# Performance work log

Hardware: AMD Instinct MI355X
Metric: run time of the kernel (lower is better)

The kernel has to match this reference:

```python
import jax, jax.numpy as jnp
import numpy as np
from jax.scipy.linalg import expm

D = 512      # d_model
S = 3        # num_scales
BATCH = 256
H = 8        # attention heads
HD = D // H  # head dim


def layernorm(x, g, b, eps=1e-5):
    m = jnp.mean(x, axis=-1, keepdims=True)
    v = jnp.var(x, axis=-1, keepdims=True)
    return (x - m) / jnp.sqrt(v + eps) * g + b


def setup_inputs() -> dict:
    key = jax.random.key(0)
    ks = jax.random.split(key, 16)
    sd = 1.0 / np.sqrt(D)
    inp = {
        'x': jax.random.normal(ks[0], (BATCH, D), jnp.float32),
        'h_prev': jax.random.normal(ks[1], (BATCH, D), jnp.float32),
        'lstm_h': jax.random.normal(ks[2], (S, BATCH, D), jnp.float32) * 0.1,
        'lstm_c': jax.random.normal(ks[3], (S, BATCH, D), jnp.float32) * 0.1,
        'A': jax.random.normal(ks[4], (D, D), jnp.float32) * sd,
        'Bm': jax.random.normal(ks[5], (D, D), jnp.float32) * sd,
        'dn_w1': jax.random.normal(ks[6], (D, D), jnp.float32) * sd,
        'dn_b1': jnp.zeros((D,), jnp.float32),
        'dn_g': jnp.ones((D,), jnp.float32),
        'dn_beta': jnp.zeros((D,), jnp.float32),
        'dn_w2': jax.random.normal(ks[7], (1, D), jnp.float32) * sd,
        'dn_b2': jnp.zeros((1,), jnp.float32),
        'lstm_wih': jax.random.normal(ks[8], (S, 4 * D, D), jnp.float32) * sd,
        'lstm_whh': jax.random.normal(ks[9], (S, 4 * D, D), jnp.float32) * sd,
        'lstm_bih': jnp.zeros((S, 4 * D), jnp.float32),
        'lstm_bhh': jnp.zeros((S, 4 * D), jnp.float32),
        'decays': jnp.linspace(0.5, 0.95, S, dtype=jnp.float32),
        'attn_in_w': jax.random.normal(ks[10], (3 * D, D), jnp.float32) * sd,
        'attn_in_b': jnp.zeros((3 * D,), jnp.float32),
        'attn_out_w': jax.random.normal(ks[11], (D, D), jnp.float32) * sd,
        'attn_out_b': jnp.zeros((D,), jnp.float32),
        'proj_w': jax.random.normal(ks[12], (D, (S + 2) * D), jnp.float32) * (1.0 / np.sqrt((S + 2) * D)),
        'proj_b': jnp.zeros((D,), jnp.float32),
        'proj_g': jnp.ones((D,), jnp.float32),
        'proj_beta': jnp.zeros((D,), jnp.float32),
    }
    return inp


def reference(x, h_prev, lstm_h, lstm_c, A, Bm, dn_w1, dn_b1, dn_g, dn_beta,
              dn_w2, dn_b2, lstm_wih, lstm_whh, lstm_bih, lstm_bhh, decays,
              attn_in_w, attn_in_b, attn_out_w, attn_out_b,
              proj_w, proj_b, proj_g, proj_beta):
    # ---- delta_net: Linear -> LayerNorm -> GELU(exact) -> Linear -> Softplus ----
    h1 = layernorm(x @ dn_w1.T + dn_b1, dn_g, dn_beta)
    h1 = jax.nn.gelu(h1, approximate=False)
    delta = jax.nn.softplus(h1 @ dn_w2.T + dn_b2)           # (B, 1)

    # ---- SSM update: h_t = expm(delta*A) h_prev + delta*B x ----
    A_disc = jax.vmap(expm)(delta[:, :, None] * A)          # (B, D, D)
    h_ssm = jnp.einsum('bij,bj->bi', A_disc, h_prev) + delta * jnp.einsum('ij,bj->bi', Bm, x)

    # ---- multi-scale LSTM cells (vectorized over scales) ----
    gates = (jnp.einsum('bd,skd->sbk', x, lstm_wih)
             + jnp.einsum('sbd,skd->sbk', lstm_h, lstm_whh)
             + (lstm_bih + lstm_bhh)[:, None, :])           # (S, B, 4D)
    gi, gf, gg, go = jnp.split(gates, 4, axis=-1)
    i_g = jax.nn.sigmoid(gi)
    f_g = jax.nn.sigmoid(gf)
    g_g = jnp.tanh(gg)
    o_g = jax.nn.sigmoid(go)
    c_raw = f_g * lstm_c + i_g * g_g                        # (S, B, D)
    h_new = o_g * jnp.tanh(c_raw)                           # (S, B, D)
    dec = decays[:, None, None]
    c_new = dec * lstm_c + (1.0 - dec) * c_raw              # (S, B, D)

    # ---- fusion attention: 1 query (h_ssm), S keys/values (h_new) ----
    Wq, Wk, Wv = jnp.split(attn_in_w, 3, axis=0)
    bq, bk, bv = jnp.split(attn_in_b, 3, axis=0)
    kv = jnp.transpose(h_new, (1, 0, 2))                    # (B, S, D)
    q = (h_ssm @ Wq.T + bq).reshape(-1, 1, H, HD).transpose(0, 2, 1, 3)   # (B,H,1,HD)
    k = (kv @ Wk.T + bk).reshape(-1, S, H, HD).transpose(0, 2, 1, 3)      # (B,H,S,HD)
    v = (kv @ Wv.T + bv).reshape(-1, S, H, HD).transpose(0, 2, 1, 3)
    scores = jnp.einsum('bhqe,bhke->bhqk', q, k) / np.sqrt(HD)
    attn = jax.nn.softmax(scores, axis=-1)
    ctx = jnp.einsum('bhqk,bhke->bhqe', attn, v)            # (B,H,1,HD)
    ctx = ctx.transpose(0, 2, 1, 3).reshape(-1, D)          # (B, D)
    fused = ctx @ attn_out_w.T + attn_out_b                 # (B, D)

    # ---- output projection over concat [h_ssm, fused, h_1..h_S] ----
    combined = jnp.concatenate([h_ssm, fused] + [h_new[i] for i in range(S)], axis=-1)
    output = layernorm(combined @ proj_w.T + proj_b, proj_g, proj_beta)
    return (output, h_ssm, h_new, c_new)
```

## Files before the change

kernel.cpp:

```cpp
#include <hip/hip_runtime.h>
#include <math.h>

#define DIM 512
#define NB 256
#define KMAX 16

using bf16x8 = __attribute__((ext_vector_type(8))) short;
using f32x4  = __attribute__((ext_vector_type(4))) float;
using float4v = __attribute__((ext_vector_type(4))) float;
using ushort4v = __attribute__((ext_vector_type(4))) unsigned short;

__device__ __forceinline__ unsigned short f2b(float f) {
    union { float f; unsigned int u; } v; v.f = f;
    unsigned int r = v.u + 0x7fffu + ((v.u >> 16) & 1u);
    return (unsigned short)(r >> 16);
}
__device__ __forceinline__ float b2f(unsigned short u) {
    union { unsigned int u; float f; } v; v.u = ((unsigned int)u) << 16;
    return v.f;
}
__device__ __forceinline__ ushort4v f2b4(float4v v) {
    ushort4v o;
    o.x = f2b(v.x); o.y = f2b(v.y); o.z = f2b(v.z); o.w = f2b(v.w);
    return o;
}

__device__ __forceinline__ void block_reduce2(float& s, float& q, float* sb1, float* sb2)
{
    int tid = threadIdx.x;
    #pragma unroll
    for (int off = 32; off > 0; off >>= 1) {
        s += __shfl_down(s, off);
        q += __shfl_down(q, off);
    }
    if ((tid & 63) == 0) { sb1[tid >> 6] = s; sb2[tid >> 6] = q; }
    __syncthreads();
    s = sb1[0] + sb1[1] + sb1[2] + sb1[3];
    q = sb2[0] + sb2[1] + sb2[2] + sb2[3];
    __syncthreads();
}

struct GemmDesc {
    const unsigned short* X;
    const unsigned short* W;
    const float* bias;
    float* Cf;
    unsigned short* Cb;
    unsigned short* Ct;
    int M, N, K, ldX, ldW, ldC, tr_row0, acc;
};
struct GemmArgs { GemmDesc d[5]; };
struct LnParams {
    const float* pre; const float* g; const float* beta;
    const float* w2; const float* b2; float* delta; float* coeff;
    int lnd_y;
};

__global__ __launch_bounds__(256) void gemm_mfma(GemmArgs args, LnParams lp)
{
    __shared__ unsigned short lsA[2][4096];
    __shared__ unsigned short lsB[2][4096];
    __shared__ float sb1[4], sb2[4];

    if ((int)blockIdx.y == lp.lnd_y) {
        int b = blockIdx.x, tid = threadIdx.x;
        int i0 = tid, i1 = tid + 256;
        float x0 = lp.pre[(size_t)b * DIM + i0];
        float x1 = lp.pre[(size_t)b * DIM + i1];
        float s = x0 + x1, q = x0 * x0 + x1 * x1;
        block_reduce2(s, q, sb1, sb2);
        float mean = s * (1.f / DIM);
        float var  = q * (1.f / DIM) - mean * mean;
        float inv  = rsqrtf(var + 1e-5f);
        float y0 = (x0 - mean) * inv * lp.g[i0] + lp.beta[i0];
        float y1 = (x1 - mean) * inv * lp.g[i1] + lp.beta[i1];
        float h0 = 0.5f * y0 * (1.f + erff(y0 * 0.70710678118654752f));
        float h1 = 0.5f * y1 * (1.f + erff(y1 * 0.70710678118654752f));
        float p = h0 * lp.w2[i0] + h1 * lp.w2[i1];
        float dummy = 0.f;
        block_reduce2(p, dummy, sb1, sb2);
        if (tid == 0) {
            float z = p + lp.b2[0];
            float d = (z > 20.f) ? z : log1pf(expf(z));
            lp.delta[b] = d;
            float c = 1.f;
            lp.coeff[b] = 1.f;
            for (int k = 1; k <= KMAX; ++k) { c *= d / (float)k; lp.coeff[k * 256 + b] = c; }
        }
        return;
    }

    GemmDesc de = args.d[blockIdx.y];
    int tn = de.N >> 6;
    int tiles = (de.M >> 6) * tn;
    int t = blockIdx.x;
    if (t >= tiles) return;
    int m0 = (t / tn) << 6;
    int n0 = (t % tn) << 6;

    int tid = threadIdx.x;
    int w = tid >> 6;
    int l = tid & 63;
    int nkt = de.K >> 6;

    int srow = w * 16 + (l >> 2);
    int schk = l & 3;
    const unsigned short* gA = de.X + (size_t)(m0 + srow) * de.ldX + schk * 8;
    const unsigned short* gB = de.W + (size_t)(n0 + srow) * de.ldW + schk * 8;
    unsigned short* lA = &lsA[0][(w * 64 + l) * 8];
    unsigned short* lB = &lsB[0][(w * 64 + l) * 8];

#define STAGE(bufi, kt)                                                          \
    do {                                                                         \
        __builtin_amdgcn_global_load_lds(                                        \
            (const __attribute__((address_space(1))) unsigned int*)(gA + (size_t)(kt) * 64), \
            (__attribute__((address_space(3))) unsigned int*)(lA + (bufi) * 4096), 16, 0, 0); \
        __builtin_amdgcn_global_load_lds(                                        \
            (const __attribute__((address_space(1))) unsigned int*)(gA + (size_t)(kt) * 64 + 32), \
            (__attribute__((address_space(3))) unsigned int*)(lA + (bufi) * 4096 + 2048), 16, 0, 0); \
        __builtin_amdgcn_global_load_lds(                                        \
            (const __attribute__((address_space(1))) unsigned int*)(gB + (size_t)(kt) * 64), \
            (__attribute__((address_space(3))) unsigned int*)(lB + (bufi) * 4096), 16, 0, 0); \
        __builtin_amdgcn_global_load_lds(                                        \
            (const __attribute__((address_space(1))) unsigned int*)(gB + (size_t)(kt) * 64 + 32), \
            (__attribute__((address_space(3))) unsigned int*)(lB + (bufi) * 4096 + 2048), 16, 0, 0); \
    } while (0)

    int mbase = (w >> 1) * 32;
    int nbase = (w & 1) * 32;

    f32x4 acc[2][2];
    #pragma unroll
    for (int i = 0; i < 2; ++i)
        #pragma unroll
        for (int j = 0; j < 2; ++j)
            acc[i][j] = (f32x4){0.f, 0.f, 0.f, 0.f};

    int kg = l >> 4;
    int fr = l & 15;
    int aslot = (mbase * 4 + fr * 4 + kg) * 8;
    int bslot = (nbase * 4 + fr * 4 + kg) * 8;

    STAGE(0, 0);

    for (int kt = 0; kt < nkt; ++kt) {
        __syncthreads();
        if (kt + 1 < nkt) STAGE((kt + 1) & 1, kt + 1);

        const unsigned short* bufA = &lsA[kt & 1][0];
        const unsigned short* bufB = &lsB[kt & 1][0];
        #pragma unroll
        for (int h = 0; h < 2; ++h) {
            bf16x8 a0 = *(const bf16x8*)(bufA + h * 2048 + aslot);
            bf16x8 a1 = *(const bf16x8*)(bufA + h * 2048 + aslot + 512);
            bf16x8 b0 = *(const bf16x8*)(bufB + h * 2048 + bslot);
            bf16x8 b1 = *(const bf16x8*)(bufB + h * 2048 + bslot + 512);
            acc[0][0] = __builtin_amdgcn_mfma_f32_16x16x32_bf16(a0, b0, acc[0][0], 0, 0, 0);
            acc[0][1] = __builtin_amdgcn_mfma_f32_16x16x32_bf16(a0, b1, acc[0][1], 0, 0, 0);
            acc[1][0] = __builtin_amdgcn_mfma_f32_16x16x32_bf16(a1, b0, acc[1][0], 0, 0, 0);
            acc[1][1] = __builtin_amdgcn_mfma_f32_16x16x32_bf16(a1, b1, acc[1][1], 0, 0, 0);
        }
    }

    #pragma unroll
    for (int mi = 0; mi < 2; ++mi) {
        #pragma unroll
        for (int ni = 0; ni < 2; ++ni) {
            int col = n0 + nbase + ni * 16 + fr;
            float bv = de.bias ? de.bias[col] : 0.f;
            #pragma unroll
            for (int r = 0; r < 4; ++r) {
                int row = m0 + mbase + mi * 16 + (l >> 4) * 4 + r;
                float v = acc[mi][ni][r] + bv;
                if (de.Cf) {
                    if (de.acc) de.Cf[(size_t)row * de.ldC + col] += v;
                    else        de.Cf[(size_t)row * de.ldC + col] = v;
                } else {
                    de.Cb[(size_t)row * de.ldC + col] = f2b(v);
                }
                if (de.Ct && row >= de.tr_row0)
                    de.Ct[(size_t)col * 512 + (row - de.tr_row0)] = f2b(v);
            }
        }
    }
#undef STAGE
}

#define NSEG 13
struct PrepArgs {
    const float* sA[NSEG]; const float* sB[NSEG]; unsigned short* dst[NSEG];
    int n4[NSEG], dRL4[NSEG], sRLA4[NSEG], sRLB4[NSEG], half4[NSEG], offA[NSEG];
    const float* A; unsigned short* ATb;
    const float* aout_w; unsigned short* aout_wT;
    const float* proj_w; const float* proj_b; const float* aout_b; float* bprime;
};
__global__ __launch_bounds__(256) void prep_kernel(PrepArgs a)
{
    __shared__ float tile[32][33];
    int bid = blockIdx.x, tid = threadIdx.x;
    if (bid < 2048) {
        const int gstride = 2048 * 256;
        int g0 = bid * 256 + tid;
        for (int seg = 0; seg < NSEG; ++seg) {
            int n4 = a.n4[seg];
            const float* sA = a.sA[seg];
            const float* sB = a.sB[seg];
            unsigned short* d = a.dst[seg];
            int dRL4 = a.dRL4[seg], sRLA4 = a.sRLA4[seg], sRLB4 = a.sRLB4[seg];
            int half4 = a.half4[seg], offA = a.offA[seg];
            for (int i = g0; i < n4; i += gstride) {
                int r = i / dRL4, c = i - r * dRL4;
                const float* src = (c < half4)
                    ? sA + ((size_t)r * sRLA4 + offA + c) * 4
                    : sB + ((size_t)r * sRLB4 + (c - half4)) * 4;
                float4v v = *(const float4v*)src;
                *(ushort4v*)(d + (size_t)i * 4) = f2b4(v);
            }
        }
    } else if (bid < 2560) {
        int t = bid - 2048;
        const float* src = (t < 256) ? a.A : a.aout_w;
        unsigned short* dst = (t < 256) ? a.ATb : a.aout_wT;
        int tt = t & 255;
        int bx = tt & 15, by = tt >> 4;
        int tx = tid & 31, ty = tid >> 5;
        #pragma unroll
        for (int i = 0; i < 32; i += 8)
            tile[ty + i][tx] = src[(size_t)(by * 32 + ty + i) * 512 + bx * 32 + tx];
        __syncthreads();
        #pragma unroll
        for (int i = 0; i < 32; i += 8)
            dst[(size_t)(bx * 32 + ty + i) * 512 + by * 32 + tx] = f2b(tile[tx][ty + i]);
    } else {
        int i = (bid - 2560) * 4 + (tid >> 6);
        int lane = tid & 63;
        float acc = 0.f;
        #pragma unroll
        for (int n = 0; n < 512; n += 64)
            acc += a.proj_w[(size_t)i * 2560 + 512 + n + lane] * a.aout_b[n + lane];
        #pragma unroll
        for (int off = 32; off > 0; off >>= 1) acc += __shfl_down(acc, off);
        if (lane == 0) a.bprime[i] = a.proj_b[i] + acc;
    }
}

__global__ void pointwise_fused(
    const float* __restrict__ Tm, const float* __restrict__ coeff,
    const float* __restrict__ h_prev, const float* __restrict__ delta,
    const float* __restrict__ Bx, float* __restrict__ hssm,
    unsigned short* __restrict__ combb,
    const float* __restrict__ gates, const float* __restrict__ bih,
    const float* __restrict__ bhh, const float* __restrict__ cin,
    const float* __restrict__ decays,
    float* __restrict__ hout, float* __restrict__ cout)
{
    int idx4 = blockIdx.x * 256 + threadIdx.x;
    int base = idx4 * 4;
    if (base < 131072) {
        int b = base >> 9, i = base & 511;
        const float* Tr = Tm + (size_t)b * (KMAX * DIM) + i;
        float4v a = *(const float4v*)(h_prev + base);
        #pragma unroll
        for (int k = 1; k <= KMAX; ++k) {
            float c = coeff[k * 256 + b];
            float4v t = *(const float4v*)(Tr + (size_t)(k - 1) * DIM);
            a.x += c * t.x; a.y += c * t.y; a.z += c * t.z; a.w += c * t.w;
        }
        float dl = delta[b];
        float4v bx = *(const float4v*)(Bx + base);
        a.x += dl * bx.x; a.y += dl * bx.y; a.z += dl * bx.z; a.w += dl * bx.w;
        *(float4v*)(hssm + base) = a;
        *(ushort4v*)(combb + (size_t)b * 2560 + i) = f2b4(a);
    } else {
        int i2 = base - 131072;
        int s = i2 / (NB * DIM);
        int r = i2 - s * (NB * DIM);
        int b = r >> 9, d = r & 511;
        const float* gr = gates + (size_t)s * 524288 + (size_t)b * 2048 + d;
        const float* bi = bih + s * 2048 + d;
        const float* bh = bhh + s * 2048 + d;
        float4v gi = *(const float4v*)(gr);
        float4v gf = *(const float4v*)(gr + 512);
        float4v gg = *(const float4v*)(gr + 1024);
        float4v go = *(const float4v*)(gr + 1536);
        float4v bi0 = *(const float4v*)(bi),       bh0 = *(const float4v*)(bh);
        float4v bi1 = *(const float4v*)(bi + 512), bh1 = *(const float4v*)(bh + 512);
        float4v bi2 = *(const float4v*)(bi + 1024),bh2 = *(const float4v*)(bh + 1024);
        float4v bi3 = *(const float4v*)(bi + 1536),bh3 = *(const float4v*)(bh + 1536);
        float4v c = *(const float4v*)(cin + i2);
        float dec = decays[s];
        float4v hn, cn;
        #pragma unroll
        for (int j = 0; j < 4; ++j) {
            float vgi = ((const float*)&gi)[j] + ((const float*)&bi0)[j] + ((const float*)&bh0)[j];
            float vgf = ((const float*)&gf)[j] + ((const float*)&bi1)[j] + ((const float*)&bh1)[j];
            float vgg = ((const float*)&gg)[j] + ((const float*)&bi2)[j] + ((const float*)&bh2)[j];
            float vgo = ((const float*)&go)[j] + ((const float*)&bi3)[j] + ((const float*)&bh3)[j];
            float ig = 1.f / (1.f + expf(-vgi));
            float fg = 1.f / (1.f + expf(-vgf));
            float g_ = tanhf(vgg);
            float og = 1.f / (1.f + expf(-vgo));
            float cc = ((const float*)&c)[j];
            float craw = fg * cc + ig * g_;
            ((float*)&hn)[j] = og * tanhf(craw);
            ((float*)&cn)[j] = dec * cc + (1.f - dec) * craw;
        }
        *(float4v*)(hout + i2) = hn;
        *(float4v*)(cout + i2) = cn;
        *(ushort4v*)(combb + (size_t)b * 2560 + 512 + s * 512 + d) = f2b4(hn);
    }
}

__global__ __launch_bounds__(128) void attn_kernel(
    const unsigned short* __restrict__ qb, const unsigned short* __restrict__ kvb,
    unsigned short* __restrict__ combb)
{
    int b = blockIdx.x, t = threadIdx.x;
    int h = t >> 4, sub = (t & 15) * 4;
    int col = h * 64 + sub;
    ushort4v q4 = *(const ushort4v*)(qb + (size_t)b * 512 + col);
    float qf[4] = { b2f(q4.x), b2f(q4.y), b2f(q4.z), b2f(q4.w) };
    float p[3];
    ushort4v k4[3], v4[3];
    #pragma unroll
    for (int s = 0; s < 3; ++s) {
        k4[s] = *(const ushort4v*)(kvb + (size_t)s * 262144 + (size_t)b * 1024 + col);
        v4[s] = *(const ushort4v*)(kvb + (size_t)s * 262144 + (size_t)b * 1024 + 512 + col);
        p[s] = qf[0] * b2f(k4[s].x) + qf[1] * b2f(k4[s].y)
             + qf[2] * b2f(k4[s].z) + qf[3] * b2f(k4[s].w);
    }
    #pragma unroll
    for (int off = 1; off < 16; off <<= 1) {
        p[0] += __shfl_xor(p[0], off);
        p[1] += __shfl_xor(p[1], off);
        p[2] += __shfl_xor(p[2], off);
    }
    const float scale = 0.125f;
    float p0 = p[0] * scale, p1 = p[1] * scale, p2 = p[2] * scale;
    float m = fmaxf(p0, fmaxf(p1, p2));
    float w0 = expf(p0 - m), w1 = expf(p1 - m), w2 = expf(p2 - m);
    float invs = 1.f / (w0 + w1 + w2);
    float4v ctx;
    ((float*)&ctx)[0] = (w0 * b2f(v4[0].x) + w1 * b2f(v4[1].x) + w2 * b2f(v4[2].x)) * invs;
    ((float*)&ctx)[1] = (w0 * b2f(v4[0].y) + w1 * b2f(v4[1].y) + w2 * b2f(v4[2].y)) * invs;
    ((float*)&ctx)[2] = (w0 * b2f(v4[0].z) + w1 * b2f(v4[1].z) + w2 * b2f(v4[2].z)) * invs;
    ((float*)&ctx)[3] = (w0 * b2f(v4[0].w) + w1 * b2f(v4[1].w) + w2 * b2f(v4[2].w)) * invs;
    *(ushort4v*)(combb + (size_t)b * 2560 + 2048 + col) = f2b4(ctx);
}

__global__ __launch_bounds__(256) void layernorm_k(
    const float* __restrict__ in, const float* __restrict__ g,
    const float* __restrict__ beta, float* __restrict__ outp)
{
    __shared__ float sb1[4], sb2[4];
    int b = blockIdx.x, tid = threadIdx.x;
    int i0 = tid, i1 = tid + 256;
    float x0 = in[(size_t)b * DIM + i0];
    float x1 = in[(size_t)b * DIM + i1];
    float s = x0 + x1, q = x0 * x0 + x1 * x1;
    block_reduce2(s, q, sb1, sb2);
    float mean = s * (1.f / DIM);
    float var  = q * (1.f / DIM) - mean * mean;
    float inv  = rsqrtf(var + 1e-5f);
    outp[(size_t)b * DIM + i0] = (x0 - mean) * inv * g[i0] + beta[i0];
    outp[(size_t)b * DIM + i1] = (x1 - mean) * inv * g[i1] + beta[i1];
}

extern "C" void kernel_launch(void* const* d_in, const int* in_sizes, int n_in,
                              void* d_out, int out_size, void* d_ws, size_t ws_size,
                              hipStream_t stream)
{
    const float* x        = (const float*)d_in[0];
    const float* h_prev   = (const float*)d_in[1];
    const float* lstm_h   = (const float*)d_in[2];
    const float* lstm_c   = (const float*)d_in[3];
    const float* A        = (const float*)d_in[4];
    const float* Bm       = (const float*)d_in[5];
    const float* dn_w1    = (const float*)d_in[6];
    const float* dn_b1    = (const float*)d_in[7];
    const float* dn_g     = (const float*)d_in[8];
    const float* dn_beta  = (const float*)d_in[9];
    const float* dn_w2    = (const float*)d_in[10];
    const float* dn_b2    = (const float*)d_in[11];
    const float* wih      = (const float*)d_in[12];
    const float* whh      = (const float*)d_in[13];
    const float* bih      = (const float*)d_in[14];
    const float* bhh      = (const float*)d_in[15];
    const float* decays   = (const float*)d_in[16];
    const float* ain_w    = (const float*)d_in[17];
    const float* ain_b    = (const float*)d_in[18];
    const float* aout_w   = (const float*)d_in[19];
    const float* aout_b   = (const float*)d_in[20];
    const float* proj_w   = (const float*)d_in[21];
    const float* proj_b   = (const float*)d_in[22];
    const float* proj_g   = (const float*)d_in[23];
    const float* proj_bt  = (const float*)d_in[24];

    float* out  = (float*)d_out;
    float* hssm = out + 131072;
    float* hnew = out + 262144;
    float* cnew = out + 655360;

    unsigned short* us = (unsigned short*)d_ws;
    unsigned short* hpb     = us;
    unsigned short* ATb     = us + 131072;
    unsigned short* dn_w1b  = us + 393216;
    unsigned short* Bmb     = us + 655360;
    unsigned short* ain_wb  = us + 917504;
    unsigned short* proj_wb = us + 1703936;
    unsigned short* P2b     = us + 3014656;
    unsigned short* aout_wT = us + 3276800;
    unsigned short* Pw      = us + 3538944;
    unsigned short* Qa      = us + 7733248;
    unsigned short* Qb      = us + 7995392;
    unsigned short* Wcat    = us + 8257536;
    unsigned short* Xcat    = us + 14548992;
    unsigned short* combb   = us + 15335424;
    unsigned short* qb      = us + 15990784;
    unsigned short* kvb     = us + 16121856;
    unsigned short* M2b     = us + 16908288;
    float* fbase  = (float*)(us + 17170432);
    float* pre1   = fbase;
    float* delta  = fbase + 131072;
    float* coeff  = fbase + 131328;
    float* Bx     = fbase + 135680;
    float* bprime = fbase + 266752;
    float* Tm     = fbase + 267264;
    float* gates  = fbase + 2364416;
    float* projout = pre1;

    LnParams lpOff; lpOff.pre = nullptr; lpOff.g = nullptr; lpOff.beta = nullptr;
    lpOff.w2 = nullptr; lpOff.b2 = nullptr; lpOff.delta = nullptr; lpOff.coeff = nullptr;
    lpOff.lnd_y = -1;

    PrepArgs pa;
    int sidx = 0;
    auto LIN = [&](const float* s, unsigned short* d, int n4) {
        pa.sA[sidx]=s; pa.sB[sidx]=s; pa.dst[sidx]=d; pa.n4[sidx]=n4;
        pa.dRL4[sidx]=n4; pa.sRLA4[sidx]=0; pa.sRLB4[sidx]=0;
        pa.half4[sidx]=n4; pa.offA[sidx]=0; ++sidx;
    };
    LIN(h_prev, hpb,     32768);
    LIN(A,      Pw,      65536);
    LIN(dn_w1,  dn_w1b,  65536);
    LIN(Bm,     Bmb,     65536);
    LIN(ain_w,  ain_wb,  196608);
    pa.sA[sidx]=proj_w; pa.sB[sidx]=proj_w + 1024; pa.dst[sidx]=proj_wb; pa.n4[sidx]=262144;
    pa.dRL4[sidx]=512; pa.sRLA4[sidx]=640; pa.sRLB4[sidx]=640; pa.half4[sidx]=128; pa.offA[sidx]=0; ++sidx;
    pa.sA[sidx]=proj_w; pa.sB[sidx]=proj_w; pa.dst[sidx]=P2b; pa.n4[sidx]=65536;
    pa.dRL4[sidx]=128; pa.sRLA4[sidx]=640; pa.sRLB4[sidx]=640; pa.half4[sidx]=128; pa.offA[sidx]=128; ++sidx;
    for (int s = 0; s < 3; ++s) {
        pa.sA[sidx]=wih + (size_t)s*1048576; pa.sB[sidx]=whh + (size_t)s*1048576;
        pa.dst[sidx]=Wcat + (size_t)s*2097152; pa.n4[sidx]=524288;
        pa.dRL4[sidx]=256; pa.sRLA4[sidx]=128; pa.sRLB4[sidx]=128; pa.half4[sidx]=128; pa.offA[sidx]=0; ++sidx;
    }
    for (int s = 0; s < 3; ++s) {
        pa.sA[sidx]=x; pa.sB[sidx]=lstm_h + (size_t)s*131072;
        pa.dst[sidx]=Xcat + (size_t)s*262144; pa.n4[sidx]=65536;
        pa.dRL4[sidx]=256; pa.sRLA4[sidx]=128; pa.sRLB4[sidx]=128; pa.half4[sidx]=128; pa.offA[sidx]=0; ++sidx;
    }
    pa.A = A; pa.ATb = ATb; pa.aout_w = aout_w; pa.aout_wT = aout_wT;
    pa.proj_w = proj_w; pa.proj_b = proj_b; pa.aout_b = aout_b; pa.bprime = bprime;
    prep_kernel<<<2688, 256, 0, stream>>>(pa);

    GemmArgs ga;
    ga.d[0] = { Xcat, dn_w1b, dn_b1, pre1, nullptr, nullptr, 256, 512, 512, 1024, 512, 512, 0, 0 };
    ga.d[1] = { Xcat, Bmb,    nullptr, Bx,  nullptr, nullptr, 256, 512, 512, 1024, 512, 512, 0, 0 };
    ga.d[2] = { P2b,  aout_wT, nullptr, nullptr, M2b, nullptr, 512, 512, 512, 512, 512, 512, 0, 0 };
    ga.d[3] = { Pw, ATb, nullptr, nullptr, Pw + 1*262144, Qa, 512, 512, 512, 512, 512, 512, 0, 0 };
    gemm_mfma<<<dim3(64, 4), 256, 0, stream>>>(ga, lpOff);

    LnParams lp1 = { pre1, dn_g, dn_beta, dn_w2, dn_b2, delta, coeff, 1 };
    ga.d[0] = { Pw, Qa, nullptr, nullptr, Pw + 2*262144, Qb, 1024, 512, 512, 512, 512, 512, 512, 0 };
    ga.d[1] = ga.d[0];
    gemm_mfma<<<dim3(256, 2), 256, 0, stream>>>(ga, lp1);

    ga.d[0] = { Pw, Qb, nullptr, nullptr, Pw + 4*262144, Qa, 2048, 512, 512, 512, 512, 512, 1536, 0 };
    gemm_mfma<<<dim3(256, 1), 256, 0, stream>>>(ga, lpOff);

    ga.d[0] = { Pw, Qa, nullptr, nullptr, Pw + 8*262144, nullptr, 4096, 512, 512, 512, 512, 512, 0, 0 };
    ga.d[1] = { hpb, Pw, nullptr, Tm, nullptr, nullptr, 256, 4096, 512, 512, 512, 8192, 0, 0 };
    for (int s = 0; s < 3; ++s)
        ga.d[2 + s] = { Xcat + (size_t)s * 262144, Wcat + (size_t)s * 2097152, nullptr,
                        gates + (size_t)s * 524288, nullptr, nullptr, 256, 2048, 1024, 1024, 1024, 2048, 0, 0 };
    gemm_mfma<<<dim3(512, 5), 256, 0, stream>>>(ga, lpOff);

    ga.d[0] = { hpb, Pw + 8*262144, nullptr, Tm + 4096, nullptr, nullptr, 256, 4096, 512, 512, 512, 8192, 0, 0 };
    gemm_mfma<<<dim3(256, 1), 256, 0, stream>>>(ga, lpOff);

    pointwise_fused<<<512, 256, 0, stream>>>(Tm, coeff, h_prev, delta, Bx, hssm, combb,
                                             gates, bih, bhh, lstm_c, decays, hnew, cnew);

    ga.d[0] = { combb, ain_wb, ain_b, nullptr, qb, nullptr, 256, 512, 512, 2560, 512, 512, 0, 0 };
    for (int s = 0; s < 3; ++s)
        ga.d[1 + s] = { combb + 512 + (size_t)s * 512, ain_wb + 262144, ain_b + 512,
                        nullptr, kvb + (size_t)s * 262144, nullptr, 256, 1024, 512, 2560, 512, 1024, 0, 0 };
    ga.d[4] = { combb, proj_wb, bprime, projout, nullptr, nullptr, 256, 512, 2048, 2560, 2048, 512, 0, 0 };
    gemm_mfma<<<dim3(64, 5), 256, 0, stream>>>(ga, lpOff);

    attn_kernel<<<256, 128, 0, stream>>>(qb, kvb, combb);

    ga.d[0] = { combb + 2048, M2b, nullptr, projout, nullptr, nullptr, 256, 512, 512, 2560, 512, 512, 0, 1 };
    gemm_mfma<<<dim3(32, 1), 256, 0, stream>>>(ga, lpOff);

    layernorm_k<<<256, 256, 0, stream>>>(projout, proj_g, proj_bt, out);
}
```

Before: 237.2 us.

## Truncate expm series, fuse attention tail with layernorm, regroup LSTM GEMMs

```diff
diff --git a/kernel.cpp b/kernel.cpp
--- a/kernel.cpp
+++ b/kernel.cpp
@@ -3,7 +3,7 @@
 
 #define DIM 512
 #define NB 256
-#define KMAX 16
+#define KMAX 12
 
 using bf16x8 = __attribute__((ext_vector_type(8))) short;
 using f32x4  = __attribute__((ext_vector_type(4))) float;
@@ -49,7 +49,7 @@
     unsigned short* Ct;
     int M, N, K, ldX, ldW, ldC, tr_row0, acc;
 };
-struct GemmArgs { GemmDesc d[5]; };
+struct GemmArgs { GemmDesc d[6]; };
 struct LnParams {
     const float* pre; const float* g; const float* beta;
     const float* w2; const float* b2; float* delta; float* coeff;
@@ -186,13 +186,11 @@
 #undef STAGE
 }
 
-#define NSEG 13
+#define NSEG 14
 struct PrepArgs {
     const float* sA[NSEG]; const float* sB[NSEG]; unsigned short* dst[NSEG];
     int n4[NSEG], dRL4[NSEG], sRLA4[NSEG], sRLB4[NSEG], half4[NSEG], offA[NSEG];
     const float* A; unsigned short* ATb;
-    const float* aout_w; unsigned short* aout_wT;
-    const float* proj_w; const float* proj_b; const float* aout_b; float* bprime;
 };
 __global__ __launch_bounds__(256) void prep_kernel(PrepArgs a)
 {
@@ -217,30 +215,17 @@
                 *(ushort4v*)(d + (size_t)i * 4) = f2b4(v);
             }
         }
-    } else if (bid < 2560) {
-        int t = bid - 2048;
-        const float* src = (t < 256) ? a.A : a.aout_w;
-        unsigned short* dst = (t < 256) ? a.ATb : a.aout_wT;
-        int tt = t & 255;
+    } else {
+        int tt = bid - 2048;
         int bx = tt & 15, by = tt >> 4;
         int tx = tid & 31, ty = tid >> 5;
         #pragma unroll
         for (int i = 0; i < 32; i += 8)
-            tile[ty + i][tx] = src[(size_t)(by * 32 + ty + i) * 512 + bx * 32 + tx];
+            tile[ty + i][tx] = a.A[(size_t)(by * 32 + ty + i) * 512 + bx * 32 + tx];
         __syncthreads();
         #pragma unroll
         for (int i = 0; i < 32; i += 8)
-            dst[(size_t)(bx * 32 + ty + i) * 512 + by * 32 + tx] = f2b(tile[tx][ty + i]);
-    } else {
-        int i = (bid - 2560) * 4 + (tid >> 6);
-        int lane = tid & 63;
-        float acc = 0.f;
-        #pragma unroll
-        for (int n = 0; n < 512; n += 64)
-            acc += a.proj_w[(size_t)i * 2560 + 512 + n + lane] * a.aout_b[n + lane];
-        #pragma unroll
-        for (int off = 32; off > 0; off >>= 1) acc += __shfl_down(acc, off);
-        if (lane == 0) a.bprime[i] = a.proj_b[i] + acc;
+            a.ATb[(size_t)(bx * 32 + ty + i) * 512 + by * 32 + tx] = f2b(tile[tx][ty + i]);
     }
 }
 
@@ -270,7 +255,7 @@
         float4v bx = *(const float4v*)(Bx + base);
         a.x += dl * bx.x; a.y += dl * bx.y; a.z += dl * bx.z; a.w += dl * bx.w;
         *(float4v*)(hssm + base) = a;
-        *(ushort4v*)(combb + (size_t)b * 2560 + i) = f2b4(a);
+        *(ushort4v*)(combb + (size_t)b * 2048 + i) = f2b4(a);
     } else {
         int i2 = base - 131072;
         int s = i2 / (NB * DIM);
@@ -283,10 +268,10 @@
         float4v gf = *(const float4v*)(gr + 512);
         float4v gg = *(const float4v*)(gr + 1024);
         float4v go = *(const float4v*)(gr + 1536);
-        float4v bi0 = *(const float4v*)(bi),       bh0 = *(const float4v*)(bh);
-        float4v bi1 = *(const float4v*)(bi + 512), bh1 = *(const float4v*)(bh + 512);
-        float4v bi2 = *(const float4v*)(bi + 1024),bh2 = *(const float4v*)(bh + 1024);
-        float4v bi3 = *(const float4v*)(bi + 1536),bh3 = *(const float4v*)(bh + 1536);
+        float4v bi0 = *(const float4v*)(bi),        bh0 = *(const float4v*)(bh);
+        float4v bi1 = *(const float4v*)(bi + 512),  bh1 = *(const float4v*)(bh + 512);
+        float4v bi2 = *(const float4v*)(bi + 1024), bh2 = *(const float4v*)(bh + 1024);
+        float4v bi3 = *(const float4v*)(bi + 1536), bh3 = *(const float4v*)(bh + 1536);
         float4v c = *(const float4v*)(cin + i2);
         float dec = decays[s];
         float4v hn, cn;
@@ -307,63 +292,93 @@
         }
         *(float4v*)(hout + i2) = hn;
         *(float4v*)(cout + i2) = cn;
-        *(ushort4v*)(combb + (size_t)b * 2560 + 512 + s * 512 + d) = f2b4(hn);
-    }
-}
-
-__global__ __launch_bounds__(128) void attn_kernel(
+        *(ushort4v*)(combb + (size_t)b * 2048 + 512 + s * 512 + d) = f2b4(hn);
+    }
+}
+
+__global__ __launch_bounds__(256) void tail_kernel(
     const unsigned short* __restrict__ qb, const unsigned short* __restrict__ kvb,
-    unsigned short* __restrict__ combb)
+    const unsigned short* __restrict__ aout_wb, const float* __restrict__ aout_b,
+    const unsigned short* __restrict__ P2b, const float* __restrict__ projA,
+    const float* __restrict__ fin_g, const float* __restrict__ fin_beta,
+    float* __restrict__ outp)
 {
-    int b = blockIdx.x, t = threadIdx.x;
-    int h = t >> 4, sub = (t & 15) * 4;
-    int col = h * 64 + sub;
-    ushort4v q4 = *(const ushort4v*)(qb + (size_t)b * 512 + col);
-    float qf[4] = { b2f(q4.x), b2f(q4.y), b2f(q4.z), b2f(q4.w) };
-    float p[3];
-    ushort4v k4[3], v4[3];
-    #pragma unroll
-    for (int s = 0; s < 3; ++s) {
-        k4[s] = *(const ushort4v*)(kvb + (size_t)s * 262144 + (size_t)b * 1024 + col);
-        v4[s] = *(const ushort4v*)(kvb + (size_t)s * 262144 + (size_t)b * 1024 + 512 + col);
-        p[s] = qf[0] * b2f(k4[s].x) + qf[1] * b2f(k4[s].y)
-             + qf[2] * b2f(k4[s].z) + qf[3] * b2f(k4[s].w);
-    }
-    #pragma unroll
-    for (int off = 1; off < 16; off <<= 1) {
-        p[0] += __shfl_xor(p[0], off);
-        p[1] += __shfl_xor(p[1], off);
-        p[2] += __shfl_xor(p[2], off);
-    }
-    const float scale = 0.125f;
-    float p0 = p[0] * scale, p1 = p[1] * scale, p2 = p[2] * scale;
-    float m = fmaxf(p0, fmaxf(p1, p2));
-    float w0 = expf(p0 - m), w1 = expf(p1 - m), w2 = expf(p2 - m);
-    float invs = 1.f / (w0 + w1 + w2);
-    float4v ctx;
-    ((float*)&ctx)[0] = (w0 * b2f(v4[0].x) + w1 * b2f(v4[1].x) + w2 * b2f(v4[2].x)) * invs;
-    ((float*)&ctx)[1] = (w0 * b2f(v4[0].y) + w1 * b2f(v4[1].y) + w2 * b2f(v4[2].y)) * invs;
-    ((float*)&ctx)[2] = (w0 * b2f(v4[0].z) + w1 * b2f(v4[1].z) + w2 * b2f(v4[2].z)) * invs;
-    ((float*)&ctx)[3] = (w0 * b2f(v4[0].w) + w1 * b2f(v4[1].w) + w2 * b2f(v4[2].w)) * invs;
-    *(ushort4v*)(combb + (size_t)b * 2560 + 2048 + col) = f2b4(ctx);
-}
-
-__global__ __launch_bounds__(256) void layernorm_k(
-    const float* __restrict__ in, const float* __restrict__ g,
-    const float* __restrict__ beta, float* __restrict__ outp)
-{
+    __shared__ float ctxs[512];
+    __shared__ float fusedl[512];
+    __shared__ float totals[512];
     __shared__ float sb1[4], sb2[4];
     int b = blockIdx.x, tid = threadIdx.x;
-    int i0 = tid, i1 = tid + 256;
-    float x0 = in[(size_t)b * DIM + i0];
-    float x1 = in[(size_t)b * DIM + i1];
+
+    if (tid < 128) {
+        int h = tid >> 4, sub = (tid & 15) * 4;
+        int col = h * 64 + sub;
+        ushort4v q4 = *(const ushort4v*)(qb + (size_t)b * 512 + col);
+        float qf[4] = { b2f(q4.x), b2f(q4.y), b2f(q4.z), b2f(q4.w) };
+        float p[3];
+        ushort4v k4[3], v4[3];
+        #pragma unroll
+        for (int s = 0; s < 3; ++s) {
+            k4[s] = *(const ushort4v*)(kvb + (size_t)s * 262144 + (size_t)b * 1024 + col);
+            v4[s] = *(const ushort4v*)(kvb + (size_t)s * 262144 + (size_t)b * 1024 + 512 + col);
+            p[s] = qf[0] * b2f(k4[s].x) + qf[1] * b2f(k4[s].y)
+                 + qf[2] * b2f(k4[s].z) + qf[3] * b2f(k4[s].w);
+        }
+        #pragma unroll
+        for (int off = 1; off < 16; off <<= 1) {
+            p[0] += __shfl_xor(p[0], off);
+            p[1] += __shfl_xor(p[1], off);
+            p[2] += __shfl_xor(p[2], off);
+        }
+        const float scale = 0.125f;
+        float p0 = p[0] * scale, p1 = p[1] * scale, p2 = p[2] * scale;
+        float m = fmaxf(p0, fmaxf(p1, p2));
+        float w0 = expf(p0 - m), w1 = expf(p1 - m), w2 = expf(p2 - m);
+        float invs = 1.f / (w0 + w1 + w2);
+        ctxs[col + 0] = (w0 * b2f(v4[0].x) + w1 * b2f(v4[1].x) + w2 * b2f(v4[2].x)) * invs;
+        ctxs[col + 1] = (w0 * b2f(v4[0].y) + w1 * b2f(v4[1].y) + w2 * b2f(v4[2].y)) * invs;
+        ctxs[col + 2] = (w0 * b2f(v4[0].z) + w1 * b2f(v4[1].z) + w2 * b2f(v4[2].z)) * invs;
+        ctxs[col + 3] = (w0 * b2f(v4[0].w) + w1 * b2f(v4[1].w) + w2 * b2f(v4[2].w)) * invs;
+    }
+    __syncthreads();
+
+    for (int jj = tid; jj < 512; jj += 256) {
+        float acc = aout_b[jj];
+        const unsigned short* wr = aout_wb + (size_t)jj * 512;
+        for (int k = 0; k < 512; k += 8) {
+            ushort4v w0 = *(const ushort4v*)(wr + k);
+            ushort4v w1 = *(const ushort4v*)(wr + k + 4);
+            acc += ctxs[k+0]*b2f(w0.x) + ctxs[k+1]*b2f(w0.y)
+                 + ctxs[k+2]*b2f(w0.z) + ctxs[k+3]*b2f(w0.w)
+                 + ctxs[k+4]*b2f(w1.x) + ctxs[k+5]*b2f(w1.y)
+                 + ctxs[k+6]*b2f(w1.z) + ctxs[k+7]*b2f(w1.w);
+        }
+        fusedl[jj] = acc;
+    }
+    __syncthreads();
+
+    for (int ii = tid; ii < 512; ii += 256) {
+        float acc = projA[(size_t)b * 512 + ii];
+        const unsigned short* pr = P2b + (size_t)ii * 512;
+        for (int j = 0; j < 512; j += 8) {
+            ushort4v w0 = *(const ushort4v*)(pr + j);
+            ushort4v w1 = *(const ushort4v*)(pr + j + 4);
+            acc += fusedl[j+0]*b2f(w0.x) + fusedl[j+1]*b2f(w0.y)
+                 + fusedl[j+2]*b2f(w0.z) + fusedl[j+3]*b2f(w0.w)
+                 + fusedl[j+4]*b2f(w1.x) + fusedl[j+5]*b2f(w1.y)
+                 + fusedl[j+6]*b2f(w1.z) + fusedl[j+7]*b2f(w1.w);
+        }
+        totals[ii] = acc;
+    }
+    __syncthreads();
+
+    float x0 = totals[tid], x1 = totals[tid + 256];
     float s = x0 + x1, q = x0 * x0 + x1 * x1;
     block_reduce2(s, q, sb1, sb2);
     float mean = s * (1.f / DIM);
     float var  = q * (1.f / DIM) - mean * mean;
     float inv  = rsqrtf(var + 1e-5f);
-    outp[(size_t)b * DIM + i0] = (x0 - mean) * inv * g[i0] + beta[i0];
-    outp[(size_t)b * DIM + i1] = (x1 - mean) * inv * g[i1] + beta[i1];
+    outp[(size_t)b * DIM + tid]       = (x0 - mean) * inv * fin_g[tid]       + fin_beta[tid];
+    outp[(size_t)b * DIM + tid + 256] = (x1 - mean) * inv * fin_g[tid + 256] + fin_beta[tid + 256];
 }
 
 extern "C" void kernel_launch(void* const* d_in, const int* in_sizes, int n_in,
@@ -408,25 +423,23 @@
     unsigned short* Bmb     = us + 655360;
     unsigned short* ain_wb  = us + 917504;
     unsigned short* proj_wb = us + 1703936;
-    unsigned short* P2b     = us + 3014656;
-    unsigned short* aout_wT = us + 3276800;
-    unsigned short* Pw      = us + 3538944;
-    unsigned short* Qa      = us + 7733248;
-    unsigned short* Qb      = us + 7995392;
-    unsigned short* Wcat    = us + 8257536;
-    unsigned short* Xcat    = us + 14548992;
-    unsigned short* combb   = us + 15335424;
-    unsigned short* qb      = us + 15990784;
-    unsigned short* kvb     = us + 16121856;
-    unsigned short* M2b     = us + 16908288;
-    float* fbase  = (float*)(us + 17170432);
+    unsigned short* P2b     = us + 2752512;
+    unsigned short* aout_wb = us + 3014656;
+    unsigned short* Pw      = us + 3276800;
+    unsigned short* Qa      = us + 6422528;
+    unsigned short* Qb      = us + 6684672;
+    unsigned short* Wcat    = us + 6946816;
+    unsigned short* Xcat    = us + 13238272;
+    unsigned short* combb   = us + 14024704;
+    unsigned short* qb      = us + 14548992;
+    unsigned short* kvb     = us + 14680064;
+    float* fbase  = (float*)(us + 15466496);
     float* pre1   = fbase;
     float* delta  = fbase + 131072;
     float* coeff  = fbase + 131328;
-    float* Bx     = fbase + 135680;
-    float* bprime = fbase + 266752;
-    float* Tm     = fbase + 267264;
-    float* gates  = fbase + 2364416;
+    float* Bx     = fbase + 134656;
+    float* Tm     = fbase + 265728;
+    float* gates  = fbase + 1838592;
     float* projout = pre1;
 
     LnParams lpOff; lpOff.pre = nullptr; lpOff.g = nullptr; lpOff.beta = nullptr;
@@ -445,6 +458,7 @@
     LIN(dn_w1,  dn_w1b,  65536);
     LIN(Bm,     Bmb,     65536);
     LIN(ain_w,  ain_wb,  196608);
+    LIN(aout_w, aout_wb, 65536);
     pa.sA[sidx]=proj_w; pa.sB[sidx]=proj_w + 1024; pa.dst[sidx]=proj_wb; pa.n4[sidx]=262144;
     pa.dRL4[sidx]=512; pa.sRLA4[sidx]=640; pa.sRLB4[sidx]=640; pa.half4[sidx]=128; pa.offA[sidx]=0; ++sidx;
     pa.sA[sidx]=proj_w; pa.sB[sidx]=proj_w; pa.dst[sidx]=P2b; pa.n4[sidx]=65536;
@@ -459,49 +473,42 @@
         pa.dst[sidx]=Xcat + (size_t)s*262144; pa.n4[sidx]=65536;
         pa.dRL4[sidx]=256; pa.sRLA4[sidx]=128; pa.sRLB4[sidx]=128; pa.half4[sidx]=128; pa.offA[sidx]=0; ++sidx;
     }
-    pa.A = A; pa.ATb = ATb; pa.aout_w = aout_w; pa.aout_wT = aout_wT;
-    pa.proj_w = proj_w; pa.proj_b = proj_b; pa.aout_b = aout_b; pa.bprime = bprime;
-    prep_kernel<<<2688, 256, 0, stream>>>(pa);
+    pa.A = A; pa.ATb = ATb;
+    prep_kernel<<<2304, 256, 0, stream>>>(pa);
 
     GemmArgs ga;
     ga.d[0] = { Xcat, dn_w1b, dn_b1, pre1, nullptr, nullptr, 256, 512, 512, 1024, 512, 512, 0, 0 };
     ga.d[1] = { Xcat, Bmb,    nullptr, Bx,  nullptr, nullptr, 256, 512, 512, 1024, 512, 512, 0, 0 };
-    ga.d[2] = { P2b,  aout_wT, nullptr, nullptr, M2b, nullptr, 512, 512, 512, 512, 512, 512, 0, 0 };
-    ga.d[3] = { Pw, ATb, nullptr, nullptr, Pw + 1*262144, Qa, 512, 512, 512, 512, 512, 512, 0, 0 };
-    gemm_mfma<<<dim3(64, 4), 256, 0, stream>>>(ga, lpOff);
+    ga.d[2] = { Pw, ATb, nullptr, nullptr, Pw + 1*262144, Qa, 512, 512, 512, 512, 512, 512, 0, 0 };
+    for (int s = 0; s < 3; ++s)
+        ga.d[3 + s] = { Xcat + (size_t)s * 262144, Wcat + (size_t)s * 2097152, nullptr,
+                        gates + (size_t)s * 524288, nullptr, nullptr, 256, 2048, 1024, 1024, 1024, 2048, 0, 0 };
+    gemm_mfma<<<dim3(128, 6), 256, 0, stream>>>(ga, lpOff);
 
     LnParams lp1 = { pre1, dn_g, dn_beta, dn_w2, dn_b2, delta, coeff, 1 };
     ga.d[0] = { Pw, Qa, nullptr, nullptr, Pw + 2*262144, Qb, 1024, 512, 512, 512, 512, 512, 512, 0 };
-    ga.d[1] = ga.d[0];
     gemm_mfma<<<dim3(256, 2), 256, 0, stream>>>(ga, lp1);
 
     ga.d[0] = { Pw, Qb, nullptr, nullptr, Pw + 4*262144, Qa, 2048, 512, 512, 512, 512, 512, 1536, 0 };
     gemm_mfma<<<dim3(256, 1), 256, 0, stream>>>(ga, lpOff);
 
-    ga.d[0] = { Pw, Qa, nullptr, nullptr, Pw + 8*262144, nullptr, 4096, 512, 512, 512, 512, 512, 0, 0 };
-    ga.d[1] = { hpb, Pw, nullptr, Tm, nullptr, nullptr, 256, 4096, 512, 512, 512, 8192, 0, 0 };
-    for (int s = 0; s < 3; ++s)
-        ga.d[2 + s] = { Xcat + (size_t)s * 262144, Wcat + (size_t)s * 2097152, nullptr,
-                        gates + (size_t)s * 524288, nullptr, nullptr, 256, 2048, 1024, 1024, 1024, 2048, 0, 0 };
-    gemm_mfma<<<dim3(512, 5), 256, 0, stream>>>(ga, lpOff);
-
-    ga.d[0] = { hpb, Pw + 8*262144, nullptr, Tm + 4096, nullptr, nullptr, 256, 4096, 512, 512, 512, 8192, 0, 0 };
-    gemm_mfma<<<dim3(256, 1), 256, 0, stream>>>(ga, lpOff);
+    ga.d[0] = { Pw, Qa, nullptr, nullptr, Pw + 8*262144, nullptr, 2048, 512, 512, 512, 512, 512, 0, 0 };
+    ga.d[1] = { hpb, Pw, nullptr, Tm, nullptr, nullptr, 256, 4096, 512, 512, 512, 6144, 0, 0 };
+    gemm_mfma<<<dim3(256, 2), 256, 0, stream>>>(ga, lpOff);
+
+    ga.d[0] = { hpb, Pw + 8*262144, nullptr, Tm + 4096, nullptr, nullptr, 256, 2048, 512, 512, 512, 6144, 0, 0 };
+    gemm_mfma<<<dim3(128, 1), 256, 0, stream>>>(ga, lpOff);
 
     pointwise_fused<<<512, 256, 0, stream>>>(Tm, coeff, h_prev, delta, Bx, hssm, combb,
                                              gates, bih, bhh, lstm_c, decays, hnew, cnew);
 
-    ga.d[0] = { combb, ain_wb, ain_b, nullptr, qb, nullptr, 256, 512, 512, 2560, 512, 512, 0, 0 };
+    ga.d[0] = { combb, ain_wb, ain_b, nullptr, qb, nullptr, 256, 512, 512, 2048, 512, 512, 0, 0 };
     for (int s = 0; s < 3; ++s)
         ga.d[1 + s] = { combb + 512 + (size_t)s * 512, ain_wb + 262144, ain_b + 512,
-                        nullptr, kvb + (size_t)s * 262144, nullptr, 256, 1024, 512, 2560, 512, 1024, 0, 0 };
-    ga.d[4] = { combb, proj_wb, bprime, projout, nullptr, nullptr, 256, 512, 2048, 2560, 2048, 512, 0, 0 };
+                        nullptr, kvb + (size_t)s * 262144, nullptr, 256, 1024, 512, 2048, 512, 1024, 0, 0 };
+    ga.d[4] = { combb, proj_wb, proj_b, projout, nullptr, nullptr, 256, 512, 2048, 2048, 2048, 512, 0, 0 };
     gemm_mfma<<<dim3(64, 5), 256, 0, stream>>>(ga, lpOff);
 
-    attn_kernel<<<256, 128, 0, stream>>>(qb, kvb, combb);
-
-    ga.d[0] = { combb + 2048, M2b, nullptr, projout, nullptr, nullptr, 256, 512, 512, 2560, 512, 512, 0, 1 };
-    gemm_mfma<<<dim3(32, 1), 256, 0, stream>>>(ga, lpOff);
-
-    layernorm_k<<<256, 256, 0, stream>>>(projout, proj_g, proj_bt, out);
-}
+    tail_kernel<<<256, 256, 0, stream>>>(qb, kvb, aout_wb, aout_b, P2b, projout,
+                                         proj_g, proj_bt, out);
+}
```

After: 245.8 us. 3.6% more time.
